# Optimization experiments

Hardware: AMD Instinct MI355X
Metric: run time of the kernel (lower is better)

The kernel has to match this reference:

```python
import jax, jax.numpy as jnp
import numpy as np

N_ROWS = 100_000   # rows to encode
N_CLASSES = 1_000  # distinct classes C
N_WORDS = 8        # int32 words per string (32-char padded strings)
INT32_MIN = -(2**31)
INT32_MAX = 2**31 - 1


def setup_inputs() -> dict:
    key = jax.random.key(0)
    k_tab, k_idx = jax.random.split(key)
    # Class table: each row is a string packed into N_WORDS int32 words.
    # Random int32 rows are unique with overwhelming probability (256-bit keys).
    classes_table = jax.random.randint(
        k_tab, (N_CLASSES, N_WORDS), INT32_MIN, INT32_MAX, dtype=jnp.int32
    )
    # Every input row must be a previously-seen label: gather rows from the table.
    idx = jax.random.randint(k_idx, (N_ROWS,), 0, N_CLASSES)
    x = classes_table[idx]  # [N_ROWS, N_WORDS] int32
    return {"x": x, "classes_table": classes_table}


def reference(x, classes_table) -> jnp.ndarray:
    # torch: prod(condition_tensors == x.view(-1,1,L), dim=2).nonzero()[1]
    # Equality over all packed words == exact string match; exactly one class
    # matches each row, so argmax over the class dim recovers nonzero()[1].
    match = jnp.all(x[:, None, :] == classes_table[None, :, :], axis=2)  # [N, C] bool
    return jnp.argmax(match, axis=1).astype(jnp.int32)  # [N]
```

## Files before the change

kernel.cpp:

```cpp
#include <hip/hip_runtime.h>
#include <stdint.h>


#define N_ROWS    100000
#define N_CLASSES 1000
#define N_WORDS   8
#define TBL_SIZE  4096
#define TBL_MASK  (TBL_SIZE - 1)

__device__ __forceinline__ uint32_t hash8(int4 a, int4 b) {
    uint64_t h = 0x9E3779B97F4A7C15ull;
    uint32_t w[8] = {(uint32_t)a.x, (uint32_t)a.y, (uint32_t)a.z, (uint32_t)a.w,
                     (uint32_t)b.x, (uint32_t)b.y, (uint32_t)b.z, (uint32_t)b.w};
#pragma unroll
    for (int i = 0; i < 8; ++i) {
        h ^= w[i];
        h *= 0x100000001B3ull;
    }
    h ^= h >> 33;
    h *= 0xFF51AFD7ED558CCDull;
    h ^= h >> 33;
    return (uint32_t)h;
}

__global__ void build_table_kernel(const int* __restrict__ tab,
                                   int* __restrict__ ht) {
    int c = blockIdx.x * blockDim.x + threadIdx.x;
    if (c >= N_CLASSES) return;
    const int4* t4 = (const int4*)(tab + (size_t)c * N_WORDS);
    int4 a = t4[0];
    int4 b = t4[1];
    uint32_t h = hash8(a, b) & TBL_MASK;
    while (atomicCAS(&ht[h], -1, c) != -1) {
        h = (h + 1) & TBL_MASK;
    }
}

__global__ void encode_kernel(const int* __restrict__ x,
                              const int* __restrict__ tab,
                              const int* __restrict__ ht,
                              int* __restrict__ out) {
    int r = blockIdx.x * blockDim.x + threadIdx.x;
    if (r >= N_ROWS) return;
    const int4* x4 = (const int4*)(x + (size_t)r * N_WORDS);
    int4 a = x4[0];
    int4 b = x4[1];
    uint32_t h = hash8(a, b) & TBL_MASK;
    int res = 0;
    while (true) {
        int c = ht[h];
        if (c < 0) { res = 0; break; }
        const int4* t4 = (const int4*)(tab + (size_t)c * N_WORDS);
        int4 ta = t4[0];
        int4 tb = t4[1];
        if (ta.x == a.x && ta.y == a.y && ta.z == a.z && ta.w == a.w &&
            tb.x == b.x && tb.y == b.y && tb.z == b.z && tb.w == b.w) {
            res = c;
            break;
        }
        h = (h + 1) & TBL_MASK;
    }
    out[r] = res;
}

extern "C" void kernel_launch(void* const* d_in, const int* in_sizes, int n_in,
                              void* d_out, int out_size, void* d_ws, size_t ws_size,
                              hipStream_t stream) {
    const int* x   = (const int*)d_in[0];
    const int* tab = (const int*)d_in[1];
    int* out = (int*)d_out;
    int* ht  = (int*)d_ws;

    hipMemsetAsync(ht, 0xFF, TBL_SIZE * sizeof(int), stream);

    build_table_kernel<<<(N_CLASSES + 255) / 256, 256, 0, stream>>>(tab, ht);
    encode_kernel<<<(N_ROWS + 255) / 256, 256, 0, stream>>>(x, tab, ht, out);
}
```

Baseline: 63.52 us.

## Fuse hash-table build and encode into one kernel with per-block shared-memory table

Removes the memset and the separate build kernel. Each block now builds its own 4096-entry hash table and a copy of the class table in shared memory, then encodes two rows per thread with probes served from LDS instead of global memory. This drops two extra launches and serialization points, but every one of the ~196 blocks redoes the 1000-class build with LDS atomics. The 48KB of shared memory per block also limits occupancy.

```diff
diff --git a/kernel.cpp b/kernel.cpp
--- a/kernel.cpp
+++ b/kernel.cpp
@@ -7,6 +7,10 @@
 #define N_WORDS   8
 #define TBL_SIZE  4096
 #define TBL_MASK  (TBL_SIZE - 1)
+#define BLOCK     256
+#define ROWS_PER_THREAD 2
+#define ROWS_PER_BLOCK  (BLOCK * ROWS_PER_THREAD)
+#define NBLOCKS   ((N_ROWS + ROWS_PER_BLOCK - 1) / ROWS_PER_BLOCK)
 
 __device__ __forceinline__ uint32_t hash8(int4 a, int4 b) {
     uint64_t h = 0x9E3779B97F4A7C15ull;
@@ -23,44 +27,54 @@
     return (uint32_t)h;
 }
 
-__global__ void build_table_kernel(const int* __restrict__ tab,
-                                   int* __restrict__ ht) {
-    int c = blockIdx.x * blockDim.x + threadIdx.x;
-    if (c >= N_CLASSES) return;
-    const int4* t4 = (const int4*)(tab + (size_t)c * N_WORDS);
-    int4 a = t4[0];
-    int4 b = t4[1];
-    uint32_t h = hash8(a, b) & TBL_MASK;
-    while (atomicCAS(&ht[h], -1, c) != -1) {
-        h = (h + 1) & TBL_MASK;
+__global__ __launch_bounds__(BLOCK) void encode_fused(
+        const int* __restrict__ x,
+        const int* __restrict__ tab,
+        int* __restrict__ out) {
+    __shared__ int ht[TBL_SIZE];
+    __shared__ int ctab[N_CLASSES * N_WORDS];
+
+    const int t = threadIdx.x;
+
+#pragma unroll
+    for (int i = t; i < TBL_SIZE; i += BLOCK) ht[i] = -1;
+    __syncthreads();
+
+    for (int c = t; c < N_CLASSES; c += BLOCK) {
+        const int4* t4 = (const int4*)(tab + (size_t)c * N_WORDS);
+        int4 a = t4[0];
+        int4 b = t4[1];
+        ((int4*)ctab)[c * 2]     = a;
+        ((int4*)ctab)[c * 2 + 1] = b;
+        uint32_t h = hash8(a, b) & TBL_MASK;
+        while (atomicCAS(&ht[h], -1, c) != -1) h = (h + 1) & TBL_MASK;
     }
-}
+    __syncthreads();
 
-__global__ void encode_kernel(const int* __restrict__ x,
-                              const int* __restrict__ tab,
-                              const int* __restrict__ ht,
-                              int* __restrict__ out) {
-    int r = blockIdx.x * blockDim.x + threadIdx.x;
-    if (r >= N_ROWS) return;
-    const int4* x4 = (const int4*)(x + (size_t)r * N_WORDS);
-    int4 a = x4[0];
-    int4 b = x4[1];
-    uint32_t h = hash8(a, b) & TBL_MASK;
-    int res = 0;
-    while (true) {
-        int c = ht[h];
-        if (c < 0) { res = 0; break; }
-        const int4* t4 = (const int4*)(tab + (size_t)c * N_WORDS);
-        int4 ta = t4[0];
-        int4 tb = t4[1];
-        if (ta.x == a.x && ta.y == a.y && ta.z == a.z && ta.w == a.w &&
-            tb.x == b.x && tb.y == b.y && tb.z == b.z && tb.w == b.w) {
-            res = c;
-            break;
+    const int base = blockIdx.x * ROWS_PER_BLOCK + t;
+#pragma unroll
+    for (int i = 0; i < ROWS_PER_THREAD; ++i) {
+        int r = base + i * BLOCK;
+        if (r >= N_ROWS) continue;
+        const int4* x4 = (const int4*)(x + (size_t)r * N_WORDS);
+        int4 a = x4[0];
+        int4 b = x4[1];
+        uint32_t h = hash8(a, b) & TBL_MASK;
+        int res = 0;
+        while (true) {
+            int c = ht[h];
+            if (c < 0) { res = 0; break; }
+            int4 ta = ((const int4*)ctab)[c * 2];
+            int4 tb = ((const int4*)ctab)[c * 2 + 1];
+            if (ta.x == a.x && ta.y == a.y && ta.z == a.z && ta.w == a.w &&
+                tb.x == b.x && tb.y == b.y && tb.z == b.z && tb.w == b.w) {
+                res = c;
+                break;
+            }
+            h = (h + 1) & TBL_MASK;
         }
-        h = (h + 1) & TBL_MASK;
+        out[r] = res;
     }
-    out[r] = res;
 }
 
 extern "C" void kernel_launch(void* const* d_in, const int* in_sizes, int n_in,
@@ -69,10 +83,6 @@
     const int* x   = (const int*)d_in[0];
     const int* tab = (const int*)d_in[1];
     int* out = (int*)d_out;
-    int* ht  = (int*)d_ws;
 
-    hipMemsetAsync(ht, 0xFF, TBL_SIZE * sizeof(int), stream);
-
-    build_table_kernel<<<(N_CLASSES + 255) / 256, 256, 0, stream>>>(tab, ht);
-    encode_kernel<<<(N_ROWS + 255) / 256, 256, 0, stream>>>(x, tab, ht, out);
+    encode_fused<<<NBLOCKS, BLOCK, 0, stream>>>(x, tab, out);
 }
```

New measurement: 61.17 us. 1.04x faster.
